# Optimization experiments

Hardware: AMD Instinct MI355X
Metric: run time of the kernel (lower is better)

## Reference

```python
import jax, jax.numpy as jnp
import numpy as np
import math

EMBED_DIM = 1024
NUM_HEADS = 16
HEAD_DIM = EMBED_DIM // NUM_HEADS
B, S = 2, 2048


def setup_inputs() -> dict:
    key = jax.random.key(0)
    ks = jax.random.split(key, 5)
    scale = 1.0 / math.sqrt(EMBED_DIM)
    x = jax.random.normal(ks[0], (B, S, EMBED_DIM), dtype=jnp.float32)
    W_q = jax.random.normal(ks[1], (EMBED_DIM, EMBED_DIM), dtype=jnp.float32) * scale
    W_k = jax.random.normal(ks[2], (EMBED_DIM, EMBED_DIM), dtype=jnp.float32) * scale
    W_v = jax.random.normal(ks[3], (EMBED_DIM, EMBED_DIM), dtype=jnp.float32) * scale
    W_o = jax.random.normal(ks[4], (EMBED_DIM, EMBED_DIM), dtype=jnp.float32) * scale
    # causal mask: True = masked out (matches torch masked_fill semantics)
    mask = jnp.triu(jnp.ones((S, S), dtype=bool), k=1)
    return {"x": x, "mask": mask, "W_q": W_q, "W_k": W_k, "W_v": W_v, "W_o": W_o}


def _split_heads(x):
    b, s, _ = x.shape
    return x.reshape(b, s, NUM_HEADS, HEAD_DIM).transpose(0, 2, 1, 3)  # [b,h,s,hd]


def reference(x, mask, W_q, W_k, W_v, W_o):
    # torch nn.Linear(bias=False): y = x @ W.T
    Q = _split_heads(x @ W_q.T)
    K = _split_heads(x @ W_k.T)
    V = _split_heads(x @ W_v.T)
    scale = 1.0 / math.sqrt(HEAD_DIM)
    scores = jnp.einsum("bhqd,bhkd->bhqk", Q, K) * scale  # [b,h,s,s]
    scores = jnp.where(mask[None, None, :, :], -jnp.inf, scores)
    weights = jax.nn.softmax(scores, axis=-1)
    out = jnp.einsum("bhqk,bhkd->bhqd", weights, V)
    out = out.transpose(0, 2, 1, 3).reshape(x.shape[0], x.shape[1], EMBED_DIM)
    return out @ W_o.T
```

## Files before the change

### kernel.cpp

```cpp
#include <hip/hip_runtime.h>
#include <hip/hip_bf16.h>

typedef short bf16x8 __attribute__((ext_vector_type(8)));
typedef unsigned short u16x8 __attribute__((ext_vector_type(8)));
typedef unsigned short u16x4 __attribute__((ext_vector_type(4)));
typedef float f32x4 __attribute__((ext_vector_type(4)));

typedef unsigned int __attribute__((address_space(1))) gu32;
typedef unsigned int __attribute__((address_space(3))) lu32;

#define MFMA16(a, b, c) __builtin_amdgcn_mfma_f32_16x16x32_bf16((a), (b), (c), 0, 0, 0)

constexpr int SEQ = 2048;
constexpr int NH = 16;
constexpr int NTOK = 2 * SEQ;

__device__ __forceinline__ float bf2f(unsigned short u) {
  union { unsigned int i; float f; } v; v.i = ((unsigned int)u) << 16; return v.f;
}
__device__ __forceinline__ unsigned short f2bf(float f) {
  __hip_bfloat16 h = __float2bfloat16(f);
  return __builtin_bit_cast(unsigned short, h);
}
__device__ __forceinline__ unsigned int pkbf_trunc(float hi, float lo) {
  return __builtin_amdgcn_perm(__builtin_bit_cast(unsigned int, hi),
                               __builtin_bit_cast(unsigned int, lo), 0x07060302u);
}
__device__ __forceinline__ u16x8 cvt8(const float* __restrict__ p) {
  f32x4 a = *(const f32x4*)p;
  f32x4 b = *(const f32x4*)(p + 4);
  u16x8 r;
#pragma unroll
  for (int j = 0; j < 4; j++) { r[j] = f2bf(a[j]); r[4 + j] = f2bf(b[j]); }
  return r;
}

__global__ __launch_bounds__(256) void cvt_all(
    const float* __restrict__ x, const float* __restrict__ wq, const float* __restrict__ wk,
    const float* __restrict__ wv, const float* __restrict__ wo,
    unsigned short* __restrict__ Xb, unsigned short* __restrict__ Wb) {
  const int z = blockIdx.y;
  const float* src = (z == 0) ? x : (z == 1) ? wq : (z == 2) ? wk : (z == 3) ? wv : wo;
  unsigned short* dst = (z == 0) ? Xb : Wb + (size_t)(z - 1) * 1024 * 1024;
  const int n = (z == 0) ? NTOK * 1024 : 1024 * 1024;
  for (int i = (blockIdx.x * 256 + threadIdx.x) * 8; i < n; i += gridDim.x * 256 * 8)
    *(u16x8*)(dst + i) = cvt8(src + i);
}

template <int ROWS, int NWAVE>
__device__ __forceinline__ void stage_glds(const unsigned short* __restrict__ gbase,
                                           int rstride,
                                           unsigned short* __restrict__ lds,
                                           int wid, int lane) {
  constexpr int ISS = ROWS * 8 / (NWAVE * 64);
#pragma unroll
  for (int t = 0; t < ISS; ++t) {
    const int slot = (wid * ISS + t) * 64 + lane;
    const int row = slot >> 3;
    const int c8 = (slot & 7) ^ (row & 7);
    const unsigned short* gp = gbase + (size_t)row * rstride + c8 * 8;
    unsigned short* lp = lds + (size_t)(wid * ISS + t) * 512;
    __builtin_amdgcn_global_load_lds((const gu32*)gp, (lu32*)lp, 16, 0, 0);
  }
}

__device__ __forceinline__ bf16x8 frag_ld(const unsigned short* __restrict__ lds, int row, int c8) {
  const int slot = row * 8 + (c8 ^ (row & 7));
  return *(const bf16x8*)(lds + slot * 8);
}

template <int BM, int BN, int LDC, bool CF32>
__global__ __launch_bounds__(256) void gemm_lds(
    const unsigned short* __restrict__ A,
    const unsigned short* __restrict__ B,
    void* __restrict__ Cv) {
  constexpr int K = 1024;
  constexpr int MI = BM / 32, NI = BN / 32;

  __shared__ __align__(16) unsigned short As[BM * 64];
  __shared__ __align__(16) unsigned short Bs[BN * 64];

  const int tid = threadIdx.x;
  const int wid = tid >> 6;
  const int lane = tid & 63;
  const int quad = lane >> 4;
  const int c16 = lane & 15;
  const int wrow = wid >> 1, wcol = wid & 1;

  const int m0 = blockIdx.x * BM;
  const int n0 = blockIdx.y * BN;

  f32x4 acc[MI][NI];
#pragma unroll
  for (int i = 0; i < MI; i++)
#pragma unroll
    for (int j = 0; j < NI; j++) acc[i][j] = f32x4{0.f, 0.f, 0.f, 0.f};

  for (int kb = 0; kb < K; kb += 64) {
    __syncthreads();
    stage_glds<BM, 4>(A + (size_t)m0 * K + kb, K, As, wid, lane);
    stage_glds<BN, 4>(B + (size_t)n0 * K + kb, K, Bs, wid, lane);
    __syncthreads();
#pragma unroll
    for (int ks = 0; ks < 2; ++ks) {
      bf16x8 af[MI], bfr[NI];
#pragma unroll
      for (int i = 0; i < MI; i++)
        af[i] = frag_ld(As, wrow * (BM / 2) + i * 16 + c16, ks * 4 + quad);
#pragma unroll
      for (int j = 0; j < NI; j++)
        bfr[j] = frag_ld(Bs, wcol * (BN / 2) + j * 16 + c16, ks * 4 + quad);
#pragma unroll
      for (int i = 0; i < MI; i++)
#pragma unroll
        for (int j = 0; j < NI; j++) acc[i][j] = MFMA16(af[i], bfr[j], acc[i][j]);
    }
  }

#pragma unroll
  for (int i = 0; i < MI; i++) {
#pragma unroll
    for (int j = 0; j < NI; j++) {
      int row = m0 + wrow * (BM / 2) + i * 16 + quad * 4;
      int col = n0 + wcol * (BN / 2) + j * 16 + c16;
#pragma unroll
      for (int r = 0; r < 4; r++) {
        if constexpr (CF32) ((float*)Cv)[(size_t)(row + r) * LDC + col] = acc[i][j][r];
        else ((unsigned short*)Cv)[(size_t)(row + r) * LDC + col] = f2bf(acc[i][j][r]);
      }
    }
  }
}

__device__ __forceinline__ int vt_idx(int d, int kv) {
  int ck = kv >> 3;
  int s = ((d >> 3) ^ d) & 7;
  return d * 64 + ((ck ^ s) << 3) + (kv & 7);
}

struct AttnShared {
  unsigned short Kt[2][64 * 64];
  unsigned short Vt[2][64 * 64];
  unsigned short Pt[4][32 * 72];
};

__global__ __launch_bounds__(256) void attn_kernel(
    const unsigned short* __restrict__ QKV,
    unsigned short* __restrict__ Oa) {
  __shared__ AttnShared sh;
  const int g = blockIdx.x;
  const int phase = g >> 8;
  const int rr = g & 255;
  const int a = rr & 7;
  const int hb = rr >> 3;
  const int h = hb & 15;
  const int b = hb >> 4;
  const int t = phase ? a : (15 - a);
  const int tid = threadIdx.x;
  const int wid = tid >> 6, lane = tid & 63;
  const int quad = lane >> 4, c16 = lane & 15;
  const size_t tokbase = (size_t)b * SEQ;
  const int q0 = t * 128;
  const int nkv = 2 * t + 2;
  const int qb = q0 + wid * 32;

  bf16x8 qf[2][2];
#pragma unroll
  for (int m = 0; m < 2; ++m) {
    const unsigned short* qp = QKV + (tokbase + qb + m * 16 + c16) * 3072 + h * 64;
#pragma unroll
    for (int ks = 0; ks < 2; ++ks) {
      u16x8 u = *(const u16x8*)(qp + ks * 32 + quad * 8);
      bf16x8 tq;
#pragma unroll
      for (int j = 0; j < 8; j++) tq[j] = (short)f2bf(0.1803368801f * bf2f(u[j]));
      qf[m][ks] = tq;
    }
  }

  const unsigned short* kbase = QKV + tokbase * 3072 + 1024 + h * 64;
  const unsigned short* vbase = QKV + tokbase * 3072 + 2048 + h * 64;
  const int vkv = (tid >> 4) * 4;
  const int vd = (tid & 15) * 4;

  f32x4 o[2][4];
  float lacc[2] = {0.f, 0.f};
#pragma unroll
  for (int m = 0; m < 2; m++)
#pragma unroll
    for (int nt = 0; nt < 4; nt++) o[m][nt] = f32x4{0.f, 0.f, 0.f, 0.f};
  unsigned short* PtW = sh.Pt[wid];

  stage_glds<64, 4>(kbase, 3072, sh.Kt[0], wid, lane);
  u16x4 vr[4];
#pragma unroll
  for (int i = 0; i < 4; i++)
    vr[i] = *(const u16x4*)(vbase + (size_t)(vkv + i) * 3072 + vd);

  for (int kt = 0; kt < nkv; ++kt) {
    const int buf = kt & 1;
#pragma unroll
    for (int dd = 0; dd < 4; ++dd) {
      uint2 w;
      w.x = (unsigned int)vr[0][dd] | ((unsigned int)vr[1][dd] << 16);
      w.y = (unsigned int)vr[2][dd] | ((unsigned int)vr[3][dd] << 16);
      *(uint2*)&sh.Vt[buf][vt_idx(vd + dd, vkv)] = w;
    }
    __syncthreads();

    if (kt + 1 < nkv) {
      const size_t nofs = (size_t)(kt + 1) * 64;
      stage_glds<64, 4>(kbase + nofs * 3072, 3072, sh.Kt[buf ^ 1], wid, lane);
#pragma unroll
      for (int i = 0; i < 4; i++)
        vr[i] = *(const u16x4*)(vbase + (nofs + vkv + i) * 3072 + vd);
    }

    const unsigned short* KtB = sh.Kt[buf];
    const unsigned short* VtB = sh.Vt[buf];
    f32x4 st[2][4];
#pragma unroll
    for (int nt = 0; nt < 4; ++nt) {
      bf16x8 k0 = frag_ld(KtB, nt * 16 + c16, quad);
      bf16x8 k1 = frag_ld(KtB, nt * 16 + c16, 4 + quad);
#pragma unroll
      for (int m = 0; m < 2; ++m) {
        f32x4 acc = f32x4{-16.f, -16.f, -16.f, -16.f};
        acc = MFMA16(k0, qf[m][0], acc);
        acc = MFMA16(k1, qf[m][1], acc);
        st[m][nt] = acc;
      }
    }
    if (kt >= nkv - 2) {
      const int kv0 = kt * 64;
#pragma unroll
      for (int m = 0; m < 2; m++) {
        const int qg = qb + m * 16 + c16;
#pragma unroll
        for (int nt = 0; nt < 4; nt++)
#pragma unroll
          for (int r = 0; r < 4; r++) {
            int kg = kv0 + nt * 16 + quad * 4 + r;
            if (kg > qg) st[m][nt][r] = -1e30f;
          }
      }
    }

#pragma unroll
    for (int m = 0; m < 2; m++)
#pragma unroll
      for (int nt = 0; nt < 4; nt++) {
        float p0 = exp2f(st[m][nt][0]);
        float p1 = exp2f(st[m][nt][1]);
        float p2 = exp2f(st[m][nt][2]);
        float p3 = exp2f(st[m][nt][3]);
        lacc[m] += (p0 + p1) + (p2 + p3);
        uint2 w;
        w.x = pkbf_trunc(p1, p0);
        w.y = pkbf_trunc(p3, p2);
        *(uint2*)&PtW[(m * 16 + c16) * 72 + nt * 16 + quad * 4] = w;
      }

#pragma unroll
    for (int ks = 0; ks < 2; ++ks) {
      bf16x8 pf[2];
#pragma unroll
      for (int m = 0; m < 2; m++)
        pf[m] = *(const bf16x8*)&PtW[(m * 16 + c16) * 72 + ks * 32 + quad * 8];
#pragma unroll
      for (int nt2 = 0; nt2 < 4; ++nt2) {
        bf16x8 vf = *(const bf16x8*)&VtB[vt_idx(nt2 * 16 + c16, ks * 32 + quad * 8)];
#pragma unroll
        for (int m = 0; m < 2; m++) o[m][nt2] = MFMA16(vf, pf[m], o[m][nt2]);
      }
    }
  }

#pragma unroll
  for (int m = 0; m < 2; m++) {
    float l = lacc[m];
    l += __shfl_xor(l, 16);
    l += __shfl_xor(l, 32);
    const float linv = 1.f / l;
    const size_t row = tokbase + qb + m * 16 + c16;
#pragma unroll
    for (int nt2 = 0; nt2 < 4; nt2++) {
      uint2 w;
      w.x = (unsigned int)f2bf(o[m][nt2][0] * linv) | ((unsigned int)f2bf(o[m][nt2][1] * linv) << 16);
      w.y = (unsigned int)f2bf(o[m][nt2][2] * linv) | ((unsigned int)f2bf(o[m][nt2][3] * linv) << 16);
      *(uint2*)&Oa[row * 1024 + h * 64 + nt2 * 16 + quad * 4] = w;
    }
  }
}

template <int BM, int BN, int LDC, bool AF32, bool CF32>
__global__ __launch_bounds__(256) void gemm_bt(
    const void* __restrict__ Av, const float* __restrict__ W0, const float* __restrict__ W1,
    const float* __restrict__ W2, void* __restrict__ Cv) {
  constexpr int K = 1024;
  constexpr int LDS_LD = 72;
  constexpr int MI = BM / 32, NI = BN / 32;
  __shared__ __align__(16) unsigned short As[BM][LDS_LD];
  __shared__ __align__(16) unsigned short Bs[BN][LDS_LD];
  const int tid = threadIdx.x, wid = tid >> 6, lane = tid & 63;
  const int quad = lane >> 4, c16 = lane & 15;
  const int wrow = wid >> 1, wcol = wid & 1;
  const float* W = (blockIdx.z == 0) ? W0 : (blockIdx.z == 1 ? W1 : W2);
  const int m0 = blockIdx.y * BM, n0 = blockIdx.x * BN, cofs = blockIdx.z * 1024;
  f32x4 acc[MI][NI];
#pragma unroll
  for (int i = 0; i < MI; i++)
#pragma unroll
    for (int j = 0; j < NI; j++) acc[i][j] = f32x4{0.f, 0.f, 0.f, 0.f};
  for (int kb = 0; kb < K; kb += 64) {
    __syncthreads();
#pragma unroll
    for (int c = tid; c < BM * 8; c += 256) {
      int row = c >> 3, c8 = c & 7;
      if constexpr (AF32)
        *(u16x8*)&As[row][c8 * 8] = cvt8((const float*)Av + (size_t)(m0 + row) * K + kb + c8 * 8);
      else
        *(u16x8*)&As[row][c8 * 8] = *(const u16x8*)((const unsigned short*)Av + (size_t)(m0 + row) * K + kb + c8 * 8);
    }
#pragma unroll
    for (int c = tid; c < BN * 8; c += 256) {
      int row = c >> 3, c8 = c & 7;
      *(u16x8*)&Bs[row][c8 * 8] = cvt8(W + (size_t)(n0 + row) * K + kb + c8 * 8);
    }
    __syncthreads();
#pragma unroll
    for (int ks = 0; ks < 2; ++ks) {
      bf16x8 af[MI], bfr[NI];
#pragma unroll
      for (int i = 0; i < MI; i++)
        af[i] = *(const bf16x8*)&As[wrow * (BM / 2) + i * 16 + c16][ks * 32 + quad * 8];
#pragma unroll
      for (int j = 0; j < NI; j++)
        bfr[j] = *(const bf16x8*)&Bs[wcol * (BN / 2) + j * 16 + c16][ks * 32 + quad * 8];
#pragma unroll
      for (int i = 0; i < MI; i++)
#pragma unroll
        for (int j = 0; j < NI; j++) acc[i][j] = MFMA16(af[i], bfr[j], acc[i][j]);
    }
  }
#pragma unroll
  for (int i = 0; i < MI; i++)
#pragma unroll
    for (int j = 0; j < NI; j++) {
      int row = m0 + wrow * (BM / 2) + i * 16 + quad * 4;
      int col = n0 + wcol * (BN / 2) + j * 16 + c16 + cofs;
#pragma unroll
      for (int r = 0; r < 4; r++) {
        if constexpr (CF32) ((float*)Cv)[(size_t)(row + r) * LDC + col] = acc[i][j][r];
        else ((unsigned short*)Cv)[(size_t)(row + r) * LDC + col] = f2bf(acc[i][j][r]);
      }
    }
}

extern "C" void kernel_launch(void* const* d_in, const int* in_sizes, int n_in,
                              void* d_out, int out_size, void* d_ws, size_t ws_size,
                              hipStream_t stream) {
  const float* x = (const float*)d_in[0];
  const float* Wq = (const float*)d_in[2];
  const float* Wk = (const float*)d_in[3];
  const float* Wv = (const float*)d_in[4];
  const float* Wo = (const float*)d_in[5];
  float* out = (float*)d_out;

  unsigned short* QKV = (unsigned short*)d_ws;
  unsigned short* Wb = QKV + (size_t)NTOK * 3072;
  unsigned short* Xb = Wb + (size_t)4 * 1024 * 1024;
  unsigned short* AT = Xb;

  if (ws_size >= (size_t)40 * 1024 * 1024) {
    cvt_all<<<dim3(256, 5), 256, 0, stream>>>(x, Wq, Wk, Wv, Wo, Xb, Wb);
    gemm_lds<128, 128, 3072, false><<<dim3(32, 24), 256, 0, stream>>>(Xb, Wb, QKV);
    attn_kernel<<<dim3(512), 256, 0, stream>>>(QKV, AT);
    gemm_lds<128, 64, 1024, true><<<dim3(32, 16), 256, 0, stream>>>(
        AT, Wb + (size_t)3 * 1024 * 1024, out);
  } else {
    unsigned short* QKV2 = (unsigned short*)d_ws;
    unsigned short* AT2 = QKV2 + (size_t)NTOK * 3072;
    gemm_bt<128, 128, 3072, true, false><<<dim3(8, 32, 3), 256, 0, stream>>>(x, Wq, Wk, Wv, QKV2);
    attn_kernel<<<dim3(512), 256, 0, stream>>>(QKV2, AT2);
    gemm_bt<64, 64, 1024, false, true><<<dim3(16, 64, 1), 256, 0, stream>>>(AT2, Wo, Wo, Wo, out);
  }
}
```

Before: 198.5 us.

## Halve attention block to 64 query rows with 128 threads and 1024 blocks

Attention blocks now cover 64 query rows with two waves instead of 128 rows with four. This doubles the grid to 1024 blocks on a 3D layout and reorders blocks so the longest causal tiles go first. V staging drops to a single buffer with an extra barrier, and each thread loads eight V rows. The P tile stride changes to 70 and the causal mask is applied only on the last KV tile. The aim is better load balance and occupancy on the causal triangle, at the cost of reloading K/V once per 64 query rows instead of once per 128 and an extra sync per iteration.

After: 223.2 us. +12.5%, slower.

```diff
diff --git a/kernel.cpp b/kernel.cpp
--- a/kernel.cpp
+++ b/kernel.cpp
@@ -138,30 +138,29 @@
   return d * 64 + ((ck ^ s) << 3) + (kv & 7);
 }
 
+constexpr int PT_LD = 70;
+
 struct AttnShared {
   unsigned short Kt[2][64 * 64];
-  unsigned short Vt[2][64 * 64];
-  unsigned short Pt[4][32 * 72];
+  unsigned short Vt[64 * 64];
+  unsigned short Pt[2][32 * PT_LD];
 };
 
-__global__ __launch_bounds__(256) void attn_kernel(
+__global__ __launch_bounds__(128) void attn_kernel(
     const unsigned short* __restrict__ QKV,
     unsigned short* __restrict__ Oa) {
   __shared__ AttnShared sh;
-  const int g = blockIdx.x;
-  const int phase = g >> 8;
-  const int rr = g & 255;
-  const int a = rr & 7;
-  const int hb = rr >> 3;
-  const int h = hb & 15;
-  const int b = hb >> 4;
-  const int t = phase ? a : (15 - a);
+  const int h = blockIdx.x;
+  const int b = blockIdx.y;
+  const int zz = blockIdx.z;
+  const int a = zz & 7, q = zz >> 3;
+  const int t = (q == 0) ? (31 - a) : (q == 1) ? (16 + a) : (q == 2) ? (15 - a) : a;
   const int tid = threadIdx.x;
   const int wid = tid >> 6, lane = tid & 63;
   const int quad = lane >> 4, c16 = lane & 15;
   const size_t tokbase = (size_t)b * SEQ;
-  const int q0 = t * 128;
-  const int nkv = 2 * t + 2;
+  const int q0 = t * 64;
+  const int nkv = t + 1;
   const int qb = q0 + wid * 32;
 
   bf16x8 qf[2][2];
@@ -180,7 +179,7 @@
 
   const unsigned short* kbase = QKV + tokbase * 3072 + 1024 + h * 64;
   const unsigned short* vbase = QKV + tokbase * 3072 + 2048 + h * 64;
-  const int vkv = (tid >> 4) * 4;
+  const int vkv8 = (tid >> 4) * 8;
   const int vd = (tid & 15) * 4;
 
   f32x4 o[2][4];
@@ -191,33 +190,35 @@
     for (int nt = 0; nt < 4; nt++) o[m][nt] = f32x4{0.f, 0.f, 0.f, 0.f};
   unsigned short* PtW = sh.Pt[wid];
 
-  stage_glds<64, 4>(kbase, 3072, sh.Kt[0], wid, lane);
-  u16x4 vr[4];
-#pragma unroll
-  for (int i = 0; i < 4; i++)
-    vr[i] = *(const u16x4*)(vbase + (size_t)(vkv + i) * 3072 + vd);
+  stage_glds<64, 2>(kbase, 3072, sh.Kt[0], wid, lane);
+  u16x4 vr[8];
+#pragma unroll
+  for (int i = 0; i < 8; i++)
+    vr[i] = *(const u16x4*)(vbase + (size_t)(vkv8 + i) * 3072 + vd);
 
   for (int kt = 0; kt < nkv; ++kt) {
     const int buf = kt & 1;
-#pragma unroll
-    for (int dd = 0; dd < 4; ++dd) {
-      uint2 w;
-      w.x = (unsigned int)vr[0][dd] | ((unsigned int)vr[1][dd] << 16);
-      w.y = (unsigned int)vr[2][dd] | ((unsigned int)vr[3][dd] << 16);
-      *(uint2*)&sh.Vt[buf][vt_idx(vd + dd, vkv)] = w;
-    }
+    __syncthreads();
+#pragma unroll
+    for (int half = 0; half < 2; ++half)
+#pragma unroll
+      for (int dd = 0; dd < 4; ++dd) {
+        uint2 w;
+        w.x = (unsigned int)vr[half * 4 + 0][dd] | ((unsigned int)vr[half * 4 + 1][dd] << 16);
+        w.y = (unsigned int)vr[half * 4 + 2][dd] | ((unsigned int)vr[half * 4 + 3][dd] << 16);
+        *(uint2*)&sh.Vt[vt_idx(vd + dd, vkv8 + half * 4)] = w;
+      }
     __syncthreads();
 
     if (kt + 1 < nkv) {
       const size_t nofs = (size_t)(kt + 1) * 64;
-      stage_glds<64, 4>(kbase + nofs * 3072, 3072, sh.Kt[buf ^ 1], wid, lane);
-#pragma unroll
-      for (int i = 0; i < 4; i++)
-        vr[i] = *(const u16x4*)(vbase + (nofs + vkv + i) * 3072 + vd);
+      stage_glds<64, 2>(kbase + nofs * 3072, 3072, sh.Kt[buf ^ 1], wid, lane);
+#pragma unroll
+      for (int i = 0; i < 8; i++)
+        vr[i] = *(const u16x4*)(vbase + (nofs + vkv8 + i) * 3072 + vd);
     }
 
     const unsigned short* KtB = sh.Kt[buf];
-    const unsigned short* VtB = sh.Vt[buf];
     f32x4 st[2][4];
 #pragma unroll
     for (int nt = 0; nt < 4; ++nt) {
@@ -231,7 +232,7 @@
         st[m][nt] = acc;
       }
     }
-    if (kt >= nkv - 2) {
+    if (kt == nkv - 1) {
       const int kv0 = kt * 64;
 #pragma unroll
       for (int m = 0; m < 2; m++) {
@@ -258,7 +259,7 @@
         uint2 w;
         w.x = pkbf_trunc(p1, p0);
         w.y = pkbf_trunc(p3, p2);
-        *(uint2*)&PtW[(m * 16 + c16) * 72 + nt * 16 + quad * 4] = w;
+        *(uint2*)&PtW[(m * 16 + c16) * PT_LD + nt * 16 + quad * 4] = w;
       }
 
 #pragma unroll
@@ -266,10 +267,10 @@
       bf16x8 pf[2];
 #pragma unroll
       for (int m = 0; m < 2; m++)
-        pf[m] = *(const bf16x8*)&PtW[(m * 16 + c16) * 72 + ks * 32 + quad * 8];
+        pf[m] = *(const bf16x8*)&PtW[(m * 16 + c16) * PT_LD + ks * 32 + quad * 8];
 #pragma unroll
       for (int nt2 = 0; nt2 < 4; ++nt2) {
-        bf16x8 vf = *(const bf16x8*)&VtB[vt_idx(nt2 * 16 + c16, ks * 32 + quad * 8)];
+        bf16x8 vf = *(const bf16x8*)&sh.Vt[vt_idx(nt2 * 16 + c16, ks * 32 + quad * 8)];
 #pragma unroll
         for (int m = 0; m < 2; m++) o[m][nt2] = MFMA16(vf, pf[m], o[m][nt2]);
       }
@@ -375,14 +376,14 @@
   if (ws_size >= (size_t)40 * 1024 * 1024) {
     cvt_all<<<dim3(256, 5), 256, 0, stream>>>(x, Wq, Wk, Wv, Wo, Xb, Wb);
     gemm_lds<128, 128, 3072, false><<<dim3(32, 24), 256, 0, stream>>>(Xb, Wb, QKV);
-    attn_kernel<<<dim3(512), 256, 0, stream>>>(QKV, AT);
+    attn_kernel<<<dim3(NH, 2, 32), 128, 0, stream>>>(QKV, AT);
     gemm_lds<128, 64, 1024, true><<<dim3(32, 16), 256, 0, stream>>>(
         AT, Wb + (size_t)3 * 1024 * 1024, out);
   } else {
     unsigned short* QKV2 = (unsigned short*)d_ws;
     unsigned short* AT2 = QKV2 + (size_t)NTOK * 3072;
     gemm_bt<128, 128, 3072, true, false><<<dim3(8, 32, 3), 256, 0, stream>>>(x, Wq, Wk, Wv, QKV2);
-    attn_kernel<<<dim3(512), 256, 0, stream>>>(QKV2, AT2);
+    attn_kernel<<<dim3(NH, 2, 32), 128, 0, stream>>>(QKV2, AT2);
     gemm_bt<64, 64, 1024, false, true><<<dim3(16, 64, 1), 256, 0, stream>>>(AT2, Wo, Wo, Wo, out);
   }
 }
```
